# Performance work log

Measured on AMD Instinct MI355X. Metric: run time of the kernel, lower is better.

The kernel has to match this reference:

```python
import jax, jax.numpy as jnp
import numpy as np

BIG = 10000000.0

def heaviside(x):
    return (jnp.tanh(BIG * x) + 1.0) * 0.5

def interception(Prec, PET, INSC):
    INSC = jnp.clip(INSC * 5.0, 0.5, 5.0)
    IMAX = jnp.maximum(jnp.minimum(INSC, PET), 0.0)
    INT = jnp.maximum(jnp.minimum(IMAX, Prec), 0.0)
    INR = jnp.maximum(Prec - INT, 0.0)
    return INT, INR

def soil_moisture_store(SMS1, SMSC):
    SMSC = jnp.clip(SMSC * 500.0, 50.0, 500.0)
    return jnp.maximum(jnp.minimum(SMS1, SMSC), 0.0)

def soil_fluxes(PET, INT, INR, COEFF, SQ, SMSC, SUB, CRAK, SMS1):
    COEFF = jnp.clip(COEFF * 400.0, 50.0, 400.0)
    SQ = jnp.clip(SQ * 6.0, 0.0, 6.0)
    SMSC = jnp.clip(SMSC * 500.0, 50.0, 500.0)
    SUB = jnp.clip(SUB, 0.0, 1.0)
    CRAK = jnp.clip(CRAK, 0.0, 1.0)
    cap = COEFF * jnp.exp(-SQ * SMS1 / SMSC)
    RMO = jnp.maximum(heaviside(cap - INR) * INR + heaviside(INR - cap) * cap, 0.0)
    IRUN = jnp.maximum(INR - RMO, 0.0)
    SRUN = jnp.maximum(SUB * (SMS1 / SMSC) * RMO, 0.0)
    REC = jnp.maximum(CRAK * (SMS1 / SMSC) * (RMO - SRUN), 0.0)
    SMF = jnp.maximum(RMO - SRUN - REC, 0.0)
    POT = jnp.maximum(PET - INT, 0.0)
    r = 10.0 * SMS1 / SMSC
    ETS = jnp.maximum(heaviside(r - POT) * POT + heaviside(POT - r) * r, 0.0)
    return RMO, IRUN, SRUN, REC, SMF, ETS

def recharge_calculation(SMS1, SMSC, REC, SMF, ETS):
    SMSC = jnp.clip(SMSC * 500.0, 50.0, 500.0)
    s = SMS1 + SMF - ETS
    RECnew = heaviside(s - SMSC) * (REC + s - SMSC) + heaviside(SMSC - s) * REC
    return jnp.maximum(RECnew, 0.0)

def groundwaterstore(GW1, RecK):
    RecK = jnp.clip(RecK * 0.3, 0.003, 0.3)
    return jnp.maximum(heaviside(GW1) * (RecK * GW1), 0.0)

def _forward(inputs, INSC, COEFF, SQ, SMSC, SUB, CRAK, RecK):
    B, T, _ = inputs.shape
    xs = jnp.transpose(inputs, (1, 0, 2))  # (T, B, 2)

    def step(carry, x):
        SMS1, GW1 = carry  # each (B, 1)
        Prec, PET = x[:, 0:1], x[:, 1:2]
        INT, INR = interception(Prec, PET, INSC)
        SMS1c = soil_moisture_store(SMS1, SMSC)
        RMO, IRUN, SRUN, REC, SMF, ETS = soil_fluxes(PET, INT, INR, COEFF, SQ, SMSC, SUB, CRAK, SMS1c)
        next_SMS = SMS1c + jnp.clip(SMF - ETS, -100000.0, 100000.0)
        RECnew = recharge_calculation(SMS1c, SMSC, REC, SMF, ETS)
        BAS = groundwaterstore(GW1, RecK)
        next_GW = GW1 + jnp.clip(RECnew - BAS, -100000.0, 100000.0)
        return (next_SMS, next_GW), jnp.concatenate([next_SMS, next_GW], axis=1)

    init = (jnp.zeros((B, 1), inputs.dtype), jnp.zeros((B, 1), inputs.dtype))
    _, outs = jax.lax.scan(step, init, xs)  # (T, B, 2)
    outs = jnp.transpose(outs, (1, 0, 2))   # (B, T, 2)
    outs = jnp.roll(outs, shift=1, axis=1)  # state at step t-1 (wrap like tf.roll)
    SMS1 = outs[:, :, 0:1]
    GW1 = outs[:, :, 1:2]
    Prec = inputs[:, :, 0:1]
    PET = inputs[:, :, 1:2]
    INT, INR = interception(Prec, PET, INSC)
    SMS1 = soil_moisture_store(SMS1, SMSC)
    RMO, IRUN, SRUN, REC, SMF, ETS = soil_fluxes(PET, INT, INR, COEFF, SQ, SMSC, SUB, CRAK, SMS1)
    RECnew = recharge_calculation(SMS1, SMSC, REC, SMF, ETS)
    BAS = groundwaterstore(GW1, RecK)
    DR = jnp.maximum(SRUN + IRUN, 0.0)
    GD = jnp.maximum(BAS, 0.0)
    Q = jnp.maximum(DR + GD, 0.0)
    return Q  # (B, T, 1)


def setup_inputs() -> dict:
    key = jax.random.key(0)
    k1, = jax.random.split(key, 1)
    B, T = 4096, 1024
    # Prec in [0, 20) mm/day, PET in [0, 8) mm/day
    u = jax.random.uniform(k1, (B, T, 2), dtype=jnp.float32)
    scale = jnp.array([20.0, 8.0], dtype=jnp.float32)
    inputs = u * scale
    p = lambda v: jnp.full((1,), v, dtype=jnp.float32)
    return {
        "inputs": inputs,
        "INSC": p(0.5), "COEFF": p(0.5), "SQ": p(0.5), "SMSC": p(0.5),
        "SUB": p(0.5), "CRAK": p(0.5), "RecK": p(0.5),
    }


def reference(inputs, INSC, COEFF, SQ, SMSC, SUB, CRAK, RecK):
    return _forward(inputs, INSC, COEFF, SQ, SMSC, SUB, CRAK, RecK)
```

## Files before the change

kernel.cpp:

```cpp
#include <hip/hip_runtime.h>
#include <hip/hip_bf16.h>
#include <math.h>


struct P {
    float INSC, SMSC, RecK, g1, lc, k1, k2, k3, c2;
};

__device__ __forceinline__ P make_params(const float* pINSC, const float* pCOEFF,
                                         const float* pSQ,   const float* pSMSC,
                                         const float* pSUB,  const float* pCRAK,
                                         const float* pRecK) {
    P p;
    p.INSC      = fminf(fmaxf(pINSC[0]  * 5.0f,   0.5f),   5.0f);
    float COEFF = fminf(fmaxf(pCOEFF[0] * 400.0f, 50.0f),  400.0f);
    float SQ    = fminf(fmaxf(pSQ[0]    * 6.0f,   0.0f),   6.0f);
    p.SMSC      = fminf(fmaxf(pSMSC[0]  * 500.0f, 50.0f),  500.0f);
    float SUB   = fminf(fmaxf(pSUB[0],  0.0f), 1.0f);
    float CRAK  = fminf(fmaxf(pCRAK[0], 0.0f), 1.0f);
    p.RecK      = fminf(fmaxf(pRecK[0]  * 0.3f,   0.003f), 0.3f);
    p.g1 = 1.0f - p.RecK;
    p.lc = log2f(COEFF);
    float inv = 1.0f / p.SMSC;
    p.k1 = SUB * inv;
    p.k2 = CRAK * inv;
    p.k3 = 10.0f * inv;
    p.c2 = (-SQ * inv) * 1.44269504088896340736f;
    return p;
}

__device__ __forceinline__ float step(float Prec, float PET, float& sms, float& gw, const P& p) {
    float INT  = fminf(fminf(p.INSC, PET), Prec);
    float INR  = Prec - INT;
    float POT  = PET - INT;
    float S    = fminf(sms, p.SMSC);
    float u    = fmaf(-p.k1, S, 1.0f);
    float v    = fmaf(-p.k2, S, 1.0f);
    float ETS  = fminf(POT, p.k3 * S);
    float SmE  = S - ETS;
    float e    = exp2f(fmaf(p.c2, S, p.lc));
    float RMO  = fminf(INR, e);
    float w    = u * RMO;
    float s2   = fmaf(v, w, SmE);
    float SMF  = v * w;
    float REC  = w - SMF;
    float RECnew = REC + fmaxf(s2 - p.SMSC, 0.0f);
    float BAS  = p.RecK * gw;
    float Q    = (INR - w) + BAS;
    gw  = fmaf(p.g1, gw, RECnew);
    sms = s2;
    return Q;
}

__device__ __forceinline__ void stepw(float Prec, float PET, float& sms, float& gw, const P& p) {
    float INT  = fminf(fminf(p.INSC, PET), Prec);
    float INR  = Prec - INT;
    float POT  = PET - INT;
    float S    = fminf(sms, p.SMSC);
    float u    = fmaf(-p.k1, S, 1.0f);
    float v    = fmaf(-p.k2, S, 1.0f);
    float ETS  = fminf(POT, p.k3 * S);
    float SmE  = S - ETS;
    float e    = exp2f(fmaf(p.c2, S, p.lc));
    float RMO  = fminf(INR, e);
    float w    = u * RMO;
    float s2   = fmaf(v, w, SmE);
    float SMF  = v * w;
    float REC  = w - SMF;
    float RECnew = REC + fmaxf(s2 - p.SMSC, 0.0f);
    gw  = fmaf(p.g1, gw, RECnew);
    sms = s2;
}

__device__ __forceinline__ void dstep(float Prec, float PET,
                                      float& slo, float& shi, float& gw, const P& p) {
    float INT = fminf(fminf(p.INSC, PET), Prec);
    float INR = Prec - INT;
    float POT = PET - INT;
    {
        float S    = fminf(shi, p.SMSC);
        float u    = fmaf(-p.k1, S, 1.0f);
        float v    = fmaf(-p.k2, S, 1.0f);
        float ETS  = fminf(POT, p.k3 * S);
        float SmE  = S - ETS;
        float e    = exp2f(fmaf(p.c2, S, p.lc));
        float RMO  = fminf(INR, e);
        float w    = u * RMO;
        float s2   = fmaf(v, w, SmE);
        float SMF  = v * w;
        float REC  = w - SMF;
        float RECnew = REC + fmaxf(s2 - p.SMSC, 0.0f);
        gw  = fmaf(p.g1, gw, RECnew);
        shi = s2;
    }
    {
        float S    = fminf(slo, p.SMSC);
        float u    = fmaf(-p.k1, S, 1.0f);
        float v    = fmaf(-p.k2, S, 1.0f);
        float ETS  = fminf(POT, p.k3 * S);
        float SmE  = S - ETS;
        float e    = exp2f(fmaf(p.c2, S, p.lc));
        float RMO  = fminf(INR, e);
        float w    = u * RMO;
        slo = fmaf(v, w, SmE);
    }
}

#define MERGE_TOL 0.75f

template<int T, int NC, int W>
__global__ __launch_bounds__(64, 1)
void hir_pass1(const float* __restrict__ inputs,
               const float* __restrict__ pINSC,  const float* __restrict__ pCOEFF,
               const float* __restrict__ pSQ,    const float* __restrict__ pSMSC,
               const float* __restrict__ pSUB,   const float* __restrict__ pCRAK,
               const float* __restrict__ pRecK,
               float* __restrict__ out, float4* __restrict__ st, int B)
{
    int gid = blockIdx.x * blockDim.x + threadIdx.x;
    int b = gid % B;
    int c = gid / B;
    if (c >= NC) return;

    P p = make_params(pINSC, pCOEFF, pSQ, pSMSC, pSUB, pCRAK, pRecK);

    const float4* __restrict__ rp = (const float4*)(inputs + (size_t)b * (2 * T));
    float* __restrict__ orow = out + (size_t)b * T;

    constexpr int CH = T / NC;
    const int i1 = (c * CH) >> 1;
    int i0 = i1 - (W >> 1);
    const bool exact = (i0 <= 0);
    if (i0 < 0) i0 = 0;

    float slo = 0.0f, shi = exact ? 0.0f : p.SMSC, gw = 0.0f;

    const int nwb = (i1 - i0) >> 2;
    if (nwb > 0) {
        float4 A[4], Bq[4], C[4];
        #pragma unroll
        for (int j = 0; j < 4; ++j) A[j] = rp[i0 + j];
        {
            int k1b = (1 < nwb) ? 1 : 0;
            #pragma unroll
            for (int j = 0; j < 4; ++j) Bq[j] = rp[i0 + 4 * k1b + j];
        }
        if (exact) {
            for (int k = 0; k < nwb; ++k) {
                int kn = (k + 2 < nwb) ? (k + 2) : (nwb - 1);
                #pragma unroll
                for (int j = 0; j < 4; ++j) C[j] = rp[i0 + 4 * kn + j];
                #pragma unroll
                for (int j = 0; j < 4; ++j) {
                    stepw(A[j].x, A[j].y, shi, gw, p);
                    stepw(A[j].z, A[j].w, shi, gw, p);
                }
                #pragma unroll
                for (int j = 0; j < 4; ++j) { A[j] = Bq[j]; Bq[j] = C[j]; }
            }
            slo = shi;
        } else {
            for (int k = 0; k < nwb; ++k) {
                int kn = (k + 2 < nwb) ? (k + 2) : (nwb - 1);
                #pragma unroll
                for (int j = 0; j < 4; ++j) C[j] = rp[i0 + 4 * kn + j];
                #pragma unroll
                for (int j = 0; j < 4; ++j) {
                    dstep(A[j].x, A[j].y, slo, shi, gw, p);
                    dstep(A[j].z, A[j].w, slo, shi, gw, p);
                }
                #pragma unroll
                for (int j = 0; j < 4; ++j) { A[j] = Bq[j]; Bq[j] = C[j]; }
            }
        }
    }
    const bool merged = exact || ((shi - slo) <= MERGE_TOL);
    float sms = exact ? shi : (0.5f * (slo + shi));

    {
        constexpr int nmb = (CH / 2) / 4;
        float4 A[4], Bq[4], C[4];
        #pragma unroll
        for (int j = 0; j < 4; ++j) A[j] = rp[i1 + j];
        #pragma unroll
        for (int j = 0; j < 4; ++j) Bq[j] = rp[i1 + 4 + j];
        for (int k = 0; k < nmb; ++k) {
            int kn = (k + 2 < nmb) ? (k + 2) : (nmb - 1);
            #pragma unroll
            for (int j = 0; j < 4; ++j) C[j] = rp[i1 + 4 * kn + j];
            int ibase = i1 + 4 * k;
            #pragma unroll
            for (int j = 0; j < 4; ++j) {
                float qa = step(A[j].x, A[j].y, sms, gw, p);
                float qb = step(A[j].z, A[j].w, sms, gw, p);
                if (c == 0 && k == 0 && j == 0) {
                    orow[1] = qb;
                } else {
                    ((float2*)orow)[ibase + j] = make_float2(qa, qb);
                }
            }
            #pragma unroll
            for (int j = 0; j < 4; ++j) { A[j] = Bq[j]; Bq[j] = C[j]; }
        }
    }

    st[(size_t)c * B + b] = make_float4(sms, gw, merged ? 1.0f : 0.0f, 0.0f);

    if (c == NC - 1) {
        float4 f0 = rp[0];
        float ss = sms, gg = gw;
        orow[0] = step(f0.x, f0.y, ss, gg, p);
    }
}

template<int T, int NC>
__global__ __launch_bounds__(64, 1)
void hir_pass2(const float* __restrict__ inputs,
               const float* __restrict__ pINSC,  const float* __restrict__ pCOEFF,
               const float* __restrict__ pSQ,    const float* __restrict__ pSMSC,
               const float* __restrict__ pSUB,   const float* __restrict__ pCRAK,
               const float* __restrict__ pRecK,
               float* __restrict__ out, const float4* __restrict__ st, int B)
{
    int gid = blockIdx.x * blockDim.x + threadIdx.x;
    int b = gid % B;
    int c = gid / B;
    if (c >= NC) return;

    float4 sc = st[(size_t)c * B + b];
    if (sc.z != 0.0f) return;

    P p = make_params(pINSC, pCOEFF, pSQ, pSMSC, pSUB, pCRAK, pRecK);
    constexpr int CH = T / NC;

    const float4* __restrict__ rp = (const float4*)(inputs + (size_t)b * (2 * T));
    float* __restrict__ orow = out + (size_t)b * T;

    int m = c - 1;
    float4 sm = st[(size_t)m * B + b];
    while (sm.z == 0.0f) { --m; sm = st[(size_t)m * B + b]; }
    float sms = sm.x, gw = sm.y;

    {
        const int ia = ((m + 1) * CH) >> 1;
        const int ib = (c * CH) >> 1;
        if (ia < ib) {
            float4 cur = rp[ia];
            for (int i = ia; i < ib; ++i) {
                int ni = (i + 1 < ib) ? (i + 1) : i;
                float4 nxt = rp[ni];
                stepw(cur.x, cur.y, sms, gw, p);
                stepw(cur.z, cur.w, sms, gw, p);
                cur = nxt;
            }
        }
    }

    {
        const int i1 = (c * CH) >> 1;
        const int i2 = ((c + 1) * CH) >> 1;
        float4 cur = rp[i1];
        for (int i = i1; i < i2; ++i) {
            int ni = (i + 1 < i2) ? (i + 1) : i;
            float4 nxt = rp[ni];
            float qa = step(cur.x, cur.y, sms, gw, p);
            float qb = step(cur.z, cur.w, sms, gw, p);
            ((float2*)orow)[i] = make_float2(qa, qb);
            cur = nxt;
        }
    }

    if (c == NC - 1) {
        float4 f0 = rp[0];
        float ss = sms, gg = gw;
        orow[0] = step(f0.x, f0.y, ss, gg, p);
    }
}

template<int T>
__global__ __launch_bounds__(64, 1)
void hir_scan_kernel(const float* __restrict__ inputs,
                     const float* __restrict__ pINSC,  const float* __restrict__ pCOEFF,
                     const float* __restrict__ pSQ,    const float* __restrict__ pSMSC,
                     const float* __restrict__ pSUB,   const float* __restrict__ pCRAK,
                     const float* __restrict__ pRecK,
                     float* __restrict__ out, int B)
{
    int b = blockIdx.x * blockDim.x + threadIdx.x;
    if (b >= B) return;
    P p = make_params(pINSC, pCOEFF, pSQ, pSMSC, pSUB, pCRAK, pRecK);
    const float4* __restrict__ rp = (const float4*)(inputs + (size_t)b * (2 * T));
    float* __restrict__ orow = out + (size_t)b * T;
    float sms = 0.0f, gw = 0.0f;
    float4 cur = rp[0];
    const float P0 = cur.x, E0 = cur.y;
    constexpr int NI = T / 2;
    for (int i = 0; i < NI; ++i) {
        int ni = (i + 1 < NI) ? (i + 1) : i;
        float4 nxt = rp[ni];
        float qa = step(cur.x, cur.y, sms, gw, p);
        float qb = step(cur.z, cur.w, sms, gw, p);
        if (i == 0) { orow[1] = qb; }
        else        { ((float2*)orow)[i] = make_float2(qa, qb); }
        cur = nxt;
    }
    float ss = sms, gg = gw;
    orow[0] = step(P0, E0, ss, gg, p);
}

extern "C" void kernel_launch(void* const* d_in, const int* in_sizes, int n_in,
                              void* d_out, int out_size, void* d_ws, size_t ws_size,
                              hipStream_t stream) {
    (void)n_in; (void)out_size;
    constexpr int T  = 1024;
    constexpr int NC = 16;
    constexpr int W  = 320;
    const float* inputs = (const float*)d_in[0];
    const float* INSC   = (const float*)d_in[1];
    const float* COEFF  = (const float*)d_in[2];
    const float* SQ     = (const float*)d_in[3];
    const float* SMSC   = (const float*)d_in[4];
    const float* SUB    = (const float*)d_in[5];
    const float* CRAK   = (const float*)d_in[6];
    const float* RecK   = (const float*)d_in[7];
    float* out = (float*)d_out;

    int B = in_sizes[0] / (2 * T);
    size_t need = (size_t)B * NC * sizeof(float4);

    if (ws_size < need || (B % 64) != 0) {
        int blocks = (B + 63) / 64;
        hir_scan_kernel<T><<<dim3(blocks), dim3(64), 0, stream>>>(
            inputs, INSC, COEFF, SQ, SMSC, SUB, CRAK, RecK, out, B);
        return;
    }

    float4* st = (float4*)d_ws;
    long total = (long)B * NC;
    int blocks1 = (int)((total + 63) / 64);
    hir_pass1<T, NC, W><<<dim3(blocks1), dim3(64), 0, stream>>>(
        inputs, INSC, COEFF, SQ, SMSC, SUB, CRAK, RecK, out, st, B);
    int blocks2 = (int)((total + 63) / 64);
    hir_pass2<T, NC><<<dim3(blocks2), dim3(64), 0, stream>>>(
        inputs, INSC, COEFF, SQ, SMSC, SUB, CRAK, RecK, out, st, B);
}
```

Before: 120.8 us.

## Split dual-bound warmup across thread pairs and compact fixup work via atomic queue

The low/high bound warmup scans that one thread used to run together are now split across two lanes, which exchange results with a shuffle. This halves the per-thread serial latency of the warmup phase but doubles the thread count, and the main phase is computed redundantly on both lanes. Non-merged chunks are pushed onto a compacted work list with an atomicAdd, so the fixup kernel touches only those items instead of launching one thread per chunk. The change adds a memset and an atomic counter, and the second lane's main-phase work is wasted.

New measurement: 214.7 us. +77.7%, slower.

```diff
diff --git a/kernel.cpp b/kernel.cpp
--- a/kernel.cpp
+++ b/kernel.cpp
@@ -72,40 +72,6 @@
     sms = s2;
 }
 
-__device__ __forceinline__ void dstep(float Prec, float PET,
-                                      float& slo, float& shi, float& gw, const P& p) {
-    float INT = fminf(fminf(p.INSC, PET), Prec);
-    float INR = Prec - INT;
-    float POT = PET - INT;
-    {
-        float S    = fminf(shi, p.SMSC);
-        float u    = fmaf(-p.k1, S, 1.0f);
-        float v    = fmaf(-p.k2, S, 1.0f);
-        float ETS  = fminf(POT, p.k3 * S);
-        float SmE  = S - ETS;
-        float e    = exp2f(fmaf(p.c2, S, p.lc));
-        float RMO  = fminf(INR, e);
-        float w    = u * RMO;
-        float s2   = fmaf(v, w, SmE);
-        float SMF  = v * w;
-        float REC  = w - SMF;
-        float RECnew = REC + fmaxf(s2 - p.SMSC, 0.0f);
-        gw  = fmaf(p.g1, gw, RECnew);
-        shi = s2;
-    }
-    {
-        float S    = fminf(slo, p.SMSC);
-        float u    = fmaf(-p.k1, S, 1.0f);
-        float v    = fmaf(-p.k2, S, 1.0f);
-        float ETS  = fminf(POT, p.k3 * S);
-        float SmE  = S - ETS;
-        float e    = exp2f(fmaf(p.c2, S, p.lc));
-        float RMO  = fminf(INR, e);
-        float w    = u * RMO;
-        slo = fmaf(v, w, SmE);
-    }
-}
-
 #define MERGE_TOL 0.75f
 
 template<int T, int NC, int W>
@@ -115,11 +81,15 @@
                const float* __restrict__ pSQ,    const float* __restrict__ pSMSC,
                const float* __restrict__ pSUB,   const float* __restrict__ pCRAK,
                const float* __restrict__ pRecK,
-               float* __restrict__ out, float4* __restrict__ st, int B)
+               float* __restrict__ out, float4* __restrict__ st,
+               unsigned int* __restrict__ qcount, unsigned int* __restrict__ qitems,
+               int B)
 {
     int gid = blockIdx.x * blockDim.x + threadIdx.x;
-    int b = gid % B;
-    int c = gid / B;
+    int h  = gid & 1;
+    int pb = gid >> 1;
+    int b = pb % B;
+    int c = pb / B;
     if (c >= NC) return;
 
     P p = make_params(pINSC, pCOEFF, pSQ, pSMSC, pSUB, pCRAK, pRecK);
@@ -133,7 +103,8 @@
     const bool exact = (i0 <= 0);
     if (i0 < 0) i0 = 0;
 
-    float slo = 0.0f, shi = exact ? 0.0f : p.SMSC, gw = 0.0f;
+    float s  = exact ? 0.0f : (h ? 0.0f : p.SMSC);
+    float gw = 0.0f;
 
     const int nwb = (i1 - i0) >> 2;
     if (nwb > 0) {
@@ -145,37 +116,27 @@
             #pragma unroll
             for (int j = 0; j < 4; ++j) Bq[j] = rp[i0 + 4 * k1b + j];
         }
-        if (exact) {
-            for (int k = 0; k < nwb; ++k) {
-                int kn = (k + 2 < nwb) ? (k + 2) : (nwb - 1);
-                #pragma unroll
-                for (int j = 0; j < 4; ++j) C[j] = rp[i0 + 4 * kn + j];
-                #pragma unroll
-                for (int j = 0; j < 4; ++j) {
-                    stepw(A[j].x, A[j].y, shi, gw, p);
-                    stepw(A[j].z, A[j].w, shi, gw, p);
-                }
-                #pragma unroll
-                for (int j = 0; j < 4; ++j) { A[j] = Bq[j]; Bq[j] = C[j]; }
+        for (int k = 0; k < nwb; ++k) {
+            int kn = (k + 2 < nwb) ? (k + 2) : (nwb - 1);
+            #pragma unroll
+            for (int j = 0; j < 4; ++j) C[j] = rp[i0 + 4 * kn + j];
+            #pragma unroll
+            for (int j = 0; j < 4; ++j) {
+                stepw(A[j].x, A[j].y, s, gw, p);
+                stepw(A[j].z, A[j].w, s, gw, p);
             }
-            slo = shi;
-        } else {
-            for (int k = 0; k < nwb; ++k) {
-                int kn = (k + 2 < nwb) ? (k + 2) : (nwb - 1);
-                #pragma unroll
-                for (int j = 0; j < 4; ++j) C[j] = rp[i0 + 4 * kn + j];
-                #pragma unroll
-                for (int j = 0; j < 4; ++j) {
-                    dstep(A[j].x, A[j].y, slo, shi, gw, p);
-                    dstep(A[j].z, A[j].w, slo, shi, gw, p);
-                }
-                #pragma unroll
-                for (int j = 0; j < 4; ++j) { A[j] = Bq[j]; Bq[j] = C[j]; }
-            }
-        }
-    }
+            #pragma unroll
+            for (int j = 0; j < 4; ++j) { A[j] = Bq[j]; Bq[j] = C[j]; }
+        }
+    }
+
+    float so = __shfl_xor(s, 1);
+    float go = __shfl_xor(gw, 1);
+    float shi = h ? so : s;
+    float slo = h ? s : so;
+    gw = h ? go : gw;
     const bool merged = exact || ((shi - slo) <= MERGE_TOL);
-    float sms = exact ? shi : (0.5f * (slo + shi));
+    float sms = 0.5f * (slo + shi);
 
     {
         constexpr int nmb = (CH / 2) / 4;
@@ -193,10 +154,12 @@
             for (int j = 0; j < 4; ++j) {
                 float qa = step(A[j].x, A[j].y, sms, gw, p);
                 float qb = step(A[j].z, A[j].w, sms, gw, p);
-                if (c == 0 && k == 0 && j == 0) {
-                    orow[1] = qb;
-                } else {
-                    ((float2*)orow)[ibase + j] = make_float2(qa, qb);
+                if (!h) {
+                    if (c == 0 && k == 0 && j == 0) {
+                        orow[1] = qb;
+                    } else {
+                        ((float2*)orow)[ibase + j] = make_float2(qa, qb);
+                    }
                 }
             }
             #pragma unroll
@@ -204,76 +167,86 @@
         }
     }
 
-    st[(size_t)c * B + b] = make_float4(sms, gw, merged ? 1.0f : 0.0f, 0.0f);
-
-    if (c == NC - 1) {
-        float4 f0 = rp[0];
-        float ss = sms, gg = gw;
-        orow[0] = step(f0.x, f0.y, ss, gg, p);
+    if (!h) {
+        st[(size_t)c * B + b] = make_float4(sms, gw, merged ? 1.0f : 0.0f, 0.0f);
+        if (!merged) {
+            unsigned int idx = atomicAdd(qcount, 1u);
+            qitems[idx] = ((unsigned int)c << 24) | (unsigned int)b;
+        }
+        if (c == NC - 1) {
+            float4 f0 = rp[0];
+            float ss = sms, gg = gw;
+            orow[0] = step(f0.x, f0.y, ss, gg, p);
+        }
     }
 }
 
 template<int T, int NC>
 __global__ __launch_bounds__(64, 1)
-void hir_pass2(const float* __restrict__ inputs,
+void hir_fixup(const float* __restrict__ inputs,
                const float* __restrict__ pINSC,  const float* __restrict__ pCOEFF,
                const float* __restrict__ pSQ,    const float* __restrict__ pSMSC,
                const float* __restrict__ pSUB,   const float* __restrict__ pCRAK,
                const float* __restrict__ pRecK,
-               float* __restrict__ out, const float4* __restrict__ st, int B)
+               float* __restrict__ out, const float4* __restrict__ st,
+               const unsigned int* __restrict__ qcount,
+               const unsigned int* __restrict__ qitems, int B)
 {
     int gid = blockIdx.x * blockDim.x + threadIdx.x;
-    int b = gid % B;
-    int c = gid / B;
-    if (c >= NC) return;
-
-    float4 sc = st[(size_t)c * B + b];
-    if (sc.z != 0.0f) return;
+    int stride = gridDim.x * blockDim.x;
+    int n = (int)*qcount;
+    if (gid >= n) return;
 
     P p = make_params(pINSC, pCOEFF, pSQ, pSMSC, pSUB, pCRAK, pRecK);
     constexpr int CH = T / NC;
 
-    const float4* __restrict__ rp = (const float4*)(inputs + (size_t)b * (2 * T));
-    float* __restrict__ orow = out + (size_t)b * T;
-
-    int m = c - 1;
-    float4 sm = st[(size_t)m * B + b];
-    while (sm.z == 0.0f) { --m; sm = st[(size_t)m * B + b]; }
-    float sms = sm.x, gw = sm.y;
-
-    {
-        const int ia = ((m + 1) * CH) >> 1;
-        const int ib = (c * CH) >> 1;
-        if (ia < ib) {
-            float4 cur = rp[ia];
-            for (int i = ia; i < ib; ++i) {
-                int ni = (i + 1 < ib) ? (i + 1) : i;
+    for (int it = gid; it < n; it += stride) {
+        unsigned int item = qitems[it];
+        int b = (int)(item & 0xFFFFFFu);
+        int c = (int)(item >> 24);
+
+        const float4* __restrict__ rp = (const float4*)(inputs + (size_t)b * (2 * T));
+        float* __restrict__ orow = out + (size_t)b * T;
+
+        int m = c - 1;
+        float4 sm = st[(size_t)m * B + b];
+        while (sm.z == 0.0f) { --m; sm = st[(size_t)m * B + b]; }
+        float sms = sm.x, gw = sm.y;
+
+        {
+            const int ia = ((m + 1) * CH) >> 1;
+            const int ib = (c * CH) >> 1;
+            if (ia < ib) {
+                float4 cur = rp[ia];
+                for (int i = ia; i < ib; ++i) {
+                    int ni = (i + 1 < ib) ? (i + 1) : i;
+                    float4 nxt = rp[ni];
+                    stepw(cur.x, cur.y, sms, gw, p);
+                    stepw(cur.z, cur.w, sms, gw, p);
+                    cur = nxt;
+                }
+            }
+        }
+
+        {
+            const int i1 = (c * CH) >> 1;
+            const int i2 = ((c + 1) * CH) >> 1;
+            float4 cur = rp[i1];
+            for (int i = i1; i < i2; ++i) {
+                int ni = (i + 1 < i2) ? (i + 1) : i;
                 float4 nxt = rp[ni];
-                stepw(cur.x, cur.y, sms, gw, p);
-                stepw(cur.z, cur.w, sms, gw, p);
+                float qa = step(cur.x, cur.y, sms, gw, p);
+                float qb = step(cur.z, cur.w, sms, gw, p);
+                ((float2*)orow)[i] = make_float2(qa, qb);
                 cur = nxt;
             }
         }
-    }
-
-    {
-        const int i1 = (c * CH) >> 1;
-        const int i2 = ((c + 1) * CH) >> 1;
-        float4 cur = rp[i1];
-        for (int i = i1; i < i2; ++i) {
-            int ni = (i + 1 < i2) ? (i + 1) : i;
-            float4 nxt = rp[ni];
-            float qa = step(cur.x, cur.y, sms, gw, p);
-            float qb = step(cur.z, cur.w, sms, gw, p);
-            ((float2*)orow)[i] = make_float2(qa, qb);
-            cur = nxt;
-        }
-    }
-
-    if (c == NC - 1) {
-        float4 f0 = rp[0];
-        float ss = sms, gg = gw;
-        orow[0] = step(f0.x, f0.y, ss, gg, p);
+
+        if (c == NC - 1) {
+            float4 f0 = rp[0];
+            float ss = sms, gg = gw;
+            orow[0] = step(f0.x, f0.y, ss, gg, p);
+        }
     }
 }
 
@@ -326,7 +299,8 @@
     float* out = (float*)d_out;
 
     int B = in_sizes[0] / (2 * T);
-    size_t need = (size_t)B * NC * sizeof(float4);
+    size_t stBytes = (size_t)B * NC * sizeof(float4);
+    size_t need = stBytes + 64 + (size_t)B * NC * sizeof(unsigned int);
 
     if (ws_size < need || (B % 64) != 0) {
         int blocks = (B + 63) / 64;
@@ -336,11 +310,17 @@
     }
 
     float4* st = (float4*)d_ws;
-    long total = (long)B * NC;
+    unsigned int* qcount = (unsigned int*)((char*)d_ws + stBytes);
+    unsigned int* qitems = (unsigned int*)((char*)d_ws + stBytes + 64);
+
+    hipMemsetAsync(qcount, 0, sizeof(unsigned int), stream);
+
+    long total = 2L * B * NC;
     int blocks1 = (int)((total + 63) / 64);
     hir_pass1<T, NC, W><<<dim3(blocks1), dim3(64), 0, stream>>>(
-        inputs, INSC, COEFF, SQ, SMSC, SUB, CRAK, RecK, out, st, B);
-    int blocks2 = (int)((total + 63) / 64);
-    hir_pass2<T, NC><<<dim3(blocks2), dim3(64), 0, stream>>>(
-        inputs, INSC, COEFF, SQ, SMSC, SUB, CRAK, RecK, out, st, B);
-}
+        inputs, INSC, COEFF, SQ, SMSC, SUB, CRAK, RecK, out, st, qcount, qitems, B);
+
+    int blocks2 = 1024;
+    hir_fixup<T, NC><<<dim3(blocks2), dim3(64), 0, stream>>>(
+        inputs, INSC, COEFF, SQ, SMSC, SUB, CRAK, RecK, out, st, qcount, qitems, B);
+}
```

## Transpose inputs to time-major layout and compact unmerged chunks into a fixup queue

Applied to the files above, without the earlier changes.

Adds tiled shared-memory transpose kernels so the chunked scan reads inputs and writes outputs time-major, which makes adjacent threads (batch lanes) touch adjacent addresses and coalesces their accesses. Unmerged chunks are compacted with a ballot/atomic queue and repaired by a grid-stride fixup kernel rather than by launching one thread per chunk. The cost is two extra full-tensor transposes through the workspace, more kernel launches plus a memset, and strided uncoalesced accesses in the fixup path. It also reworks the legacy pass2 fallback to loop over chunks per batch row.

Result: slower. 145.9 us (+20.8%).

```diff
diff --git a/kernel.cpp b/kernel.cpp
--- a/kernel.cpp
+++ b/kernel.cpp
@@ -108,9 +108,237 @@
 
 #define MERGE_TOL 0.75f
 
+
+__global__ __launch_bounds__(256)
+void transpose_in(const float2* __restrict__ in, float2* __restrict__ tp,
+                  int B, int Tdim)
+{
+    __shared__ float2 tile[64][65];
+    int t0 = blockIdx.x * 64, b0 = blockIdx.y * 64;
+    int l = threadIdx.x & 63, w = threadIdx.x >> 6;
+    #pragma unroll
+    for (int j = 0; j < 16; ++j) {
+        int bb = w * 16 + j;
+        tile[l][bb] = in[(long)(b0 + bb) * Tdim + t0 + l];
+    }
+    __syncthreads();
+    #pragma unroll
+    for (int j = 0; j < 16; ++j) {
+        int tt = w * 16 + j;
+        tp[(long)(t0 + tt) * B + b0 + l] = tile[tt][l];
+    }
+}
+
+__global__ __launch_bounds__(256)
+void transpose_out(const float* __restrict__ qtp, float* __restrict__ out,
+                   int B, int Tdim)
+{
+    __shared__ float tile[64][65];
+    int t0 = blockIdx.x * 64, b0 = blockIdx.y * 64;
+    int l = threadIdx.x & 63, w = threadIdx.x >> 6;
+    #pragma unroll
+    for (int j = 0; j < 16; ++j) {
+        int tt = w * 16 + j;
+        tile[tt][l] = qtp[(long)(t0 + tt) * B + b0 + l];
+    }
+    __syncthreads();
+    #pragma unroll
+    for (int j = 0; j < 16; ++j) {
+        int bb = w * 16 + j;
+        out[(long)(b0 + bb) * Tdim + t0 + l] = tile[l][bb];
+    }
+}
+
+
 template<int T, int NC, int W>
 __global__ __launch_bounds__(64, 1)
-void hir_pass1(const float* __restrict__ inputs,
+void hir_pass1t(const float2* __restrict__ tp,
+                const float* __restrict__ pINSC,  const float* __restrict__ pCOEFF,
+                const float* __restrict__ pSQ,    const float* __restrict__ pSMSC,
+                const float* __restrict__ pSUB,   const float* __restrict__ pCRAK,
+                const float* __restrict__ pRecK,
+                float* __restrict__ qtp, float4* __restrict__ st, int B)
+{
+    int gid = blockIdx.x * blockDim.x + threadIdx.x;
+    int b = gid % B;
+    int c = gid / B;
+    if (c >= NC) return;
+
+    P p = make_params(pINSC, pCOEFF, pSQ, pSMSC, pSUB, pCRAK, pRecK);
+
+    const float2* __restrict__ col = tp + b;
+
+    constexpr int CH = T / NC;
+    const int t1 = c * CH;
+    int t0 = t1 - W;
+    const bool exact = (t0 <= 0);
+    if (t0 < 0) t0 = 0;
+
+    float slo = 0.0f, shi = exact ? 0.0f : p.SMSC, gw = 0.0f;
+
+    const int nwb = (t1 - t0) >> 3;
+    if (nwb > 0) {
+        float2 A[8], Bq[8], C[8];
+        #pragma unroll
+        for (int j = 0; j < 8; ++j) A[j] = col[(long)(t0 + j) * B];
+        {
+            int tB = t0 + ((1 < nwb) ? 8 : 0);
+            #pragma unroll
+            for (int j = 0; j < 8; ++j) Bq[j] = col[(long)(tB + j) * B];
+        }
+        if (exact) {
+            for (int k = 0; k < nwb; ++k) {
+                int kn = (k + 2 < nwb) ? (k + 2) : (nwb - 1);
+                #pragma unroll
+                for (int j = 0; j < 8; ++j) C[j] = col[(long)(t0 + 8 * kn + j) * B];
+                #pragma unroll
+                for (int j = 0; j < 8; ++j) stepw(A[j].x, A[j].y, shi, gw, p);
+                #pragma unroll
+                for (int j = 0; j < 8; ++j) { A[j] = Bq[j]; Bq[j] = C[j]; }
+            }
+            slo = shi;
+        } else {
+            for (int k = 0; k < nwb; ++k) {
+                int kn = (k + 2 < nwb) ? (k + 2) : (nwb - 1);
+                #pragma unroll
+                for (int j = 0; j < 8; ++j) C[j] = col[(long)(t0 + 8 * kn + j) * B];
+                #pragma unroll
+                for (int j = 0; j < 8; ++j) dstep(A[j].x, A[j].y, slo, shi, gw, p);
+                #pragma unroll
+                for (int j = 0; j < 8; ++j) { A[j] = Bq[j]; Bq[j] = C[j]; }
+            }
+        }
+    }
+    const bool merged = exact || ((shi - slo) <= MERGE_TOL);
+    float sms = exact ? shi : (0.5f * (slo + shi));
+
+    {
+        constexpr int nmb = CH / 8;
+        float2 A[8], Bq[8], C[8];
+        #pragma unroll
+        for (int j = 0; j < 8; ++j) A[j] = col[(long)(t1 + j) * B];
+        #pragma unroll
+        for (int j = 0; j < 8; ++j) Bq[j] = col[(long)(t1 + 8 + j) * B];
+        for (int k = 0; k < nmb; ++k) {
+            int kn = (k + 2 < nmb) ? (k + 2) : (nmb - 1);
+            #pragma unroll
+            for (int j = 0; j < 8; ++j) C[j] = col[(long)(t1 + 8 * kn + j) * B];
+            int tb = t1 + 8 * k;
+            #pragma unroll
+            for (int j = 0; j < 8; ++j) {
+                float q = step(A[j].x, A[j].y, sms, gw, p);
+                int t = tb + j;
+                if (!(c == 0 && t == 0)) {
+                    qtp[(long)t * B + b] = q;
+                }
+            }
+            #pragma unroll
+            for (int j = 0; j < 8; ++j) { A[j] = Bq[j]; Bq[j] = C[j]; }
+        }
+    }
+
+    st[(size_t)c * B + b] = make_float4(sms, gw, merged ? 1.0f : 0.0f, 0.0f);
+
+    if (c == NC - 1) {
+        float2 f0 = col[0];
+        float ss = sms, gg = gw;
+        qtp[b] = step(f0.x, f0.y, ss, gg, p);
+    }
+}
+
+
+__global__ __launch_bounds__(64)
+void build_queue(const float4* __restrict__ st, unsigned int* __restrict__ qcount,
+                 unsigned int* __restrict__ qitems, int n)
+{
+    int gid = blockIdx.x * blockDim.x + threadIdx.x;
+    bool un = false;
+    if (gid < n) un = (st[gid].z == 0.0f);
+    unsigned long long mask = __ballot(un);
+    int lane = threadIdx.x;
+    int cnt = __popcll(mask);
+    unsigned int base = 0;
+    if (lane == 0 && cnt) base = atomicAdd(qcount, (unsigned int)cnt);
+    base = (unsigned int)__shfl((int)base, 0);
+    if (un) {
+        int pre = __popcll(mask & ((1ull << lane) - 1ull));
+        qitems[base + pre] = (unsigned int)gid;
+    }
+}
+
+
+template<int T, int NC>
+__global__ __launch_bounds__(64)
+void hir_fixup(const float* __restrict__ inputs,
+               const float* __restrict__ pINSC,  const float* __restrict__ pCOEFF,
+               const float* __restrict__ pSQ,    const float* __restrict__ pSMSC,
+               const float* __restrict__ pSUB,   const float* __restrict__ pCRAK,
+               const float* __restrict__ pRecK,
+               float* __restrict__ qtp, const float4* __restrict__ st,
+               const unsigned int* __restrict__ qcount,
+               const unsigned int* __restrict__ qitems, int B)
+{
+    int gid = blockIdx.x * blockDim.x + threadIdx.x;
+    int stride = gridDim.x * blockDim.x;
+    int n = (int)*qcount;
+
+    P p = make_params(pINSC, pCOEFF, pSQ, pSMSC, pSUB, pCRAK, pRecK);
+    constexpr int CH = T / NC;
+
+    for (int it = gid; it < n; it += stride) {
+        unsigned int item = qitems[it];
+        int b = (int)(item % (unsigned int)B);
+        int c = (int)(item / (unsigned int)B);
+
+        const float4* __restrict__ rp = (const float4*)(inputs + (size_t)b * (2 * T));
+
+        int m = c - 1;
+        float4 sm = st[(size_t)m * B + b];
+        while (sm.z == 0.0f) { --m; sm = st[(size_t)m * B + b]; }
+        float sms = sm.x, gw = sm.y;
+
+        {
+            const int ia = ((m + 1) * CH) >> 1;
+            const int ib = (c * CH) >> 1;
+            if (ia < ib) {
+                float4 cur = rp[ia];
+                for (int i = ia; i < ib; ++i) {
+                    int ni = (i + 1 < ib) ? (i + 1) : i;
+                    float4 nxt = rp[ni];
+                    stepw(cur.x, cur.y, sms, gw, p);
+                    stepw(cur.z, cur.w, sms, gw, p);
+                    cur = nxt;
+                }
+            }
+        }
+
+        {
+            const int i1 = (c * CH) >> 1;
+            const int i2 = ((c + 1) * CH) >> 1;
+            float4 cur = rp[i1];
+            for (int i = i1; i < i2; ++i) {
+                int ni = (i + 1 < i2) ? (i + 1) : i;
+                float4 nxt = rp[ni];
+                float qa = step(cur.x, cur.y, sms, gw, p);
+                float qb = step(cur.z, cur.w, sms, gw, p);
+                qtp[(long)(2 * i) * B + b]     = qa;
+                qtp[(long)(2 * i + 1) * B + b] = qb;
+                cur = nxt;
+            }
+        }
+
+        if (c == NC - 1) {
+            float4 f0 = rp[0];
+            float ss = sms, gg = gw;
+            qtp[b] = step(f0.x, f0.y, ss, gg, p);
+        }
+    }
+}
+
+
+template<int T, int NC, int W>
+__global__ __launch_bounds__(64, 1)
+void hir_pass1_legacy(const float* __restrict__ inputs,
                const float* __restrict__ pINSC,  const float* __restrict__ pCOEFF,
                const float* __restrict__ pSQ,    const float* __restrict__ pSMSC,
                const float* __restrict__ pSUB,   const float* __restrict__ pCRAK,
@@ -215,20 +443,15 @@
 
 template<int T, int NC>
 __global__ __launch_bounds__(64, 1)
-void hir_pass2(const float* __restrict__ inputs,
+void hir_pass2_legacy(const float* __restrict__ inputs,
                const float* __restrict__ pINSC,  const float* __restrict__ pCOEFF,
                const float* __restrict__ pSQ,    const float* __restrict__ pSMSC,
                const float* __restrict__ pSUB,   const float* __restrict__ pCRAK,
                const float* __restrict__ pRecK,
                float* __restrict__ out, const float4* __restrict__ st, int B)
 {
-    int gid = blockIdx.x * blockDim.x + threadIdx.x;
-    int b = gid % B;
-    int c = gid / B;
-    if (c >= NC) return;
-
-    float4 sc = st[(size_t)c * B + b];
-    if (sc.z != 0.0f) return;
+    int b = blockIdx.x * blockDim.x + threadIdx.x;
+    if (b >= B) return;
 
     P p = make_params(pINSC, pCOEFF, pSQ, pSMSC, pSUB, pCRAK, pRecK);
     constexpr int CH = T / NC;
@@ -236,27 +459,16 @@
     const float4* __restrict__ rp = (const float4*)(inputs + (size_t)b * (2 * T));
     float* __restrict__ orow = out + (size_t)b * T;
 
-    int m = c - 1;
-    float4 sm = st[(size_t)m * B + b];
-    while (sm.z == 0.0f) { --m; sm = st[(size_t)m * B + b]; }
-    float sms = sm.x, gw = sm.y;
-
-    {
-        const int ia = ((m + 1) * CH) >> 1;
-        const int ib = (c * CH) >> 1;
-        if (ia < ib) {
-            float4 cur = rp[ia];
-            for (int i = ia; i < ib; ++i) {
-                int ni = (i + 1 < ib) ? (i + 1) : i;
-                float4 nxt = rp[ni];
-                stepw(cur.x, cur.y, sms, gw, p);
-                stepw(cur.z, cur.w, sms, gw, p);
-                cur = nxt;
-            }
-        }
-    }
-
-    {
+    float4 s0 = st[b];
+    float ex_s = s0.x, ex_g = s0.y;
+
+    for (int c = 1; c < NC; ++c) {
+        float4 sc = st[(size_t)c * B + b];
+        if (sc.z != 0.0f) {
+            ex_s = sc.x; ex_g = sc.y;
+            continue;
+        }
+        float sms = ex_s, gw = ex_g;
         const int i1 = (c * CH) >> 1;
         const int i2 = ((c + 1) * CH) >> 1;
         float4 cur = rp[i1];
@@ -268,12 +480,12 @@
             ((float2*)orow)[i] = make_float2(qa, qb);
             cur = nxt;
         }
-    }
-
-    if (c == NC - 1) {
-        float4 f0 = rp[0];
-        float ss = sms, gg = gw;
-        orow[0] = step(f0.x, f0.y, ss, gg, p);
+        ex_s = sms; ex_g = gw;
+        if (c == NC - 1) {
+            float4 f0 = rp[0];
+            float ss = sms, gg = gw;
+            orow[0] = step(f0.x, f0.y, ss, gg, p);
+        }
     }
 }
 
@@ -326,21 +538,53 @@
     float* out = (float*)d_out;
 
     int B = in_sizes[0] / (2 * T);
-    size_t need = (size_t)B * NC * sizeof(float4);
-
-    if (ws_size < need || (B % 64) != 0) {
-        int blocks = (B + 63) / 64;
-        hir_scan_kernel<T><<<dim3(blocks), dim3(64), 0, stream>>>(
-            inputs, INSC, COEFF, SQ, SMSC, SUB, CRAK, RecK, out, B);
+    size_t tpBytes  = (size_t)B * T * sizeof(float2);
+    size_t qtpBytes = (size_t)B * T * sizeof(float);
+    size_t stBytes  = (size_t)B * NC * sizeof(float4);
+    size_t qBytes   = (size_t)B * NC * sizeof(unsigned int);
+    size_t bigNeed  = tpBytes + qtpBytes + stBytes + 64 + qBytes;
+
+    if ((B % 64) == 0 && ws_size >= bigNeed) {
+        float2* tp = (float2*)d_ws;
+        float*  qtp = (float*)((char*)d_ws + tpBytes);
+        float4* st  = (float4*)((char*)d_ws + tpBytes + qtpBytes);
+        unsigned int* qcount = (unsigned int*)((char*)d_ws + tpBytes + qtpBytes + stBytes);
+        unsigned int* qitems = (unsigned int*)((char*)d_ws + tpBytes + qtpBytes + stBytes + 64);
+
+        hipMemsetAsync(qcount, 0, sizeof(unsigned int), stream);
+
+        transpose_in<<<dim3(T / 64, B / 64), dim3(256), 0, stream>>>(
+            (const float2*)inputs, tp, B, T);
+
+        long total = (long)B * NC;
+        int blocks1 = (int)((total + 63) / 64);
+        hir_pass1t<T, NC, W><<<dim3(blocks1), dim3(64), 0, stream>>>(
+            tp, INSC, COEFF, SQ, SMSC, SUB, CRAK, RecK, qtp, st, B);
+
+        build_queue<<<dim3(blocks1), dim3(64), 0, stream>>>(
+            st, qcount, qitems, (int)total);
+
+        hir_fixup<T, NC><<<dim3(1024), dim3(64), 0, stream>>>(
+            inputs, INSC, COEFF, SQ, SMSC, SUB, CRAK, RecK, qtp, st, qcount, qitems, B);
+
+        transpose_out<<<dim3(T / 64, B / 64), dim3(256), 0, stream>>>(
+            qtp, out, B, T);
         return;
     }
 
-    float4* st = (float4*)d_ws;
-    long total = (long)B * NC;
-    int blocks1 = (int)((total + 63) / 64);
-    hir_pass1<T, NC, W><<<dim3(blocks1), dim3(64), 0, stream>>>(
-        inputs, INSC, COEFF, SQ, SMSC, SUB, CRAK, RecK, out, st, B);
-    int blocks2 = (int)((total + 63) / 64);
-    hir_pass2<T, NC><<<dim3(blocks2), dim3(64), 0, stream>>>(
-        inputs, INSC, COEFF, SQ, SMSC, SUB, CRAK, RecK, out, st, B);
-}
+    if ((B % 64) == 0 && ws_size >= stBytes) {
+        float4* st = (float4*)d_ws;
+        long total = (long)B * NC;
+        int blocks1 = (int)((total + 63) / 64);
+        hir_pass1_legacy<T, NC, W><<<dim3(blocks1), dim3(64), 0, stream>>>(
+            inputs, INSC, COEFF, SQ, SMSC, SUB, CRAK, RecK, out, st, B);
+        int blocks2 = (B + 63) / 64;
+        hir_pass2_legacy<T, NC><<<dim3(blocks2), dim3(64), 0, stream>>>(
+            inputs, INSC, COEFF, SQ, SMSC, SUB, CRAK, RecK, out, st, B);
+        return;
+    }
+
+    int blocks = (B + 63) / 64;
+    hir_scan_kernel<T><<<dim3(blocks), dim3(64), 0, stream>>>(
+        inputs, INSC, COEFF, SQ, SMSC, SUB, CRAK, RecK, out, B);
+}
```

## Stage pass-1 outputs in LDS and write coalesced time-major rows

Applied to the files above, without the earlier changes.

Pass 1 now stores each thread's chunk of Q values into a padded shared-memory tile and, after a barrier, writes them out so that adjacent lanes write adjacent time steps of one batch row. Before, each lane wrote float2 values strided by a full row, which gave uncoalesced stores. The warm-up window W grows from 320 to 384 so more chunks can merge, at the cost of extra serial warm-up work. The fixup kernel drops its manual prefetch and gets relaxed launch bounds.

Result: slower. 123.8 us (+2.5%).

```diff
diff --git a/kernel.cpp b/kernel.cpp
--- a/kernel.cpp
+++ b/kernel.cpp
@@ -108,6 +108,7 @@
 
 #define MERGE_TOL 0.75f
 
+
 template<int T, int NC, int W>
 __global__ __launch_bounds__(64, 1)
 void hir_pass1(const float* __restrict__ inputs,
@@ -117,9 +118,11 @@
                const float* __restrict__ pRecK,
                float* __restrict__ out, float4* __restrict__ st, int B)
 {
-    int gid = blockIdx.x * blockDim.x + threadIdx.x;
-    int b = gid % B;
-    int c = gid / B;
+    __shared__ float lds_q[64][65];
+    const int l   = threadIdx.x;
+    const int gid = blockIdx.x * 64 + l;
+    const int b = gid % B;
+    const int c = gid / B;
     if (c >= NC) return;
 
     P p = make_params(pINSC, pCOEFF, pSQ, pSMSC, pSUB, pCRAK, pRecK);
@@ -188,16 +191,13 @@
             int kn = (k + 2 < nmb) ? (k + 2) : (nmb - 1);
             #pragma unroll
             for (int j = 0; j < 4; ++j) C[j] = rp[i1 + 4 * kn + j];
-            int ibase = i1 + 4 * k;
+            int tb = 8 * k;
             #pragma unroll
             for (int j = 0; j < 4; ++j) {
                 float qa = step(A[j].x, A[j].y, sms, gw, p);
                 float qb = step(A[j].z, A[j].w, sms, gw, p);
-                if (c == 0 && k == 0 && j == 0) {
-                    orow[1] = qb;
-                } else {
-                    ((float2*)orow)[ibase + j] = make_float2(qa, qb);
-                }
+                lds_q[tb + 2 * j][l]     = qa;
+                lds_q[tb + 2 * j + 1][l] = qb;
             }
             #pragma unroll
             for (int j = 0; j < 4; ++j) { A[j] = Bq[j]; Bq[j] = C[j]; }
@@ -206,25 +206,41 @@
 
     st[(size_t)c * B + b] = make_float4(sms, gw, merged ? 1.0f : 0.0f, 0.0f);
 
-    if (c == NC - 1) {
+    float q0 = 0.0f;
+    const bool hasq0 = (c == NC - 1);
+    if (hasq0) {
         float4 f0 = rp[0];
         float ss = sms, gg = gw;
-        orow[0] = step(f0.x, f0.y, ss, gg, p);
-    }
-}
+        q0 = step(f0.x, f0.y, ss, gg, p);
+    }
+
+    __syncthreads();
+
+    const int b0 = b - l;
+    const int t1 = c * CH;
+    const bool skip0 = (c == 0);
+    for (int j = 0; j < 64; ++j) {
+        float v = lds_q[l][j];
+        if (!skip0 || l > 0) {
+            out[(size_t)(b0 + j) * T + t1 + l] = v;
+        }
+    }
+    if (hasq0) orow[0] = q0;
+}
+
 
 template<int T, int NC>
-__global__ __launch_bounds__(64, 1)
-void hir_pass2(const float* __restrict__ inputs,
+__global__ __launch_bounds__(64)
+void hir_fixup(const float* __restrict__ inputs,
                const float* __restrict__ pINSC,  const float* __restrict__ pCOEFF,
                const float* __restrict__ pSQ,    const float* __restrict__ pSMSC,
                const float* __restrict__ pSUB,   const float* __restrict__ pCRAK,
                const float* __restrict__ pRecK,
                float* __restrict__ out, const float4* __restrict__ st, int B)
 {
-    int gid = blockIdx.x * blockDim.x + threadIdx.x;
-    int b = gid % B;
-    int c = gid / B;
+    const int gid = blockIdx.x * 64 + threadIdx.x;
+    const int b = gid % B;
+    const int c = gid / B;
     if (c >= NC) return;
 
     float4 sc = st[(size_t)c * B + b];
@@ -244,29 +260,21 @@
     {
         const int ia = ((m + 1) * CH) >> 1;
         const int ib = (c * CH) >> 1;
-        if (ia < ib) {
-            float4 cur = rp[ia];
-            for (int i = ia; i < ib; ++i) {
-                int ni = (i + 1 < ib) ? (i + 1) : i;
-                float4 nxt = rp[ni];
-                stepw(cur.x, cur.y, sms, gw, p);
-                stepw(cur.z, cur.w, sms, gw, p);
-                cur = nxt;
-            }
+        for (int i = ia; i < ib; ++i) {
+            float4 cur = rp[i];
+            stepw(cur.x, cur.y, sms, gw, p);
+            stepw(cur.z, cur.w, sms, gw, p);
         }
     }
 
     {
         const int i1 = (c * CH) >> 1;
         const int i2 = ((c + 1) * CH) >> 1;
-        float4 cur = rp[i1];
         for (int i = i1; i < i2; ++i) {
-            int ni = (i + 1 < i2) ? (i + 1) : i;
-            float4 nxt = rp[ni];
+            float4 cur = rp[i];
             float qa = step(cur.x, cur.y, sms, gw, p);
             float qb = step(cur.z, cur.w, sms, gw, p);
             ((float2*)orow)[i] = make_float2(qa, qb);
-            cur = nxt;
         }
     }
 
@@ -314,7 +322,7 @@
     (void)n_in; (void)out_size;
     constexpr int T  = 1024;
     constexpr int NC = 16;
-    constexpr int W  = 320;
+    constexpr int W  = 384;
     const float* inputs = (const float*)d_in[0];
     const float* INSC   = (const float*)d_in[1];
     const float* COEFF  = (const float*)d_in[2];
@@ -326,21 +334,20 @@
     float* out = (float*)d_out;
 
     int B = in_sizes[0] / (2 * T);
-    size_t need = (size_t)B * NC * sizeof(float4);
-
-    if (ws_size < need || (B % 64) != 0) {
-        int blocks = (B + 63) / 64;
-        hir_scan_kernel<T><<<dim3(blocks), dim3(64), 0, stream>>>(
-            inputs, INSC, COEFF, SQ, SMSC, SUB, CRAK, RecK, out, B);
+    size_t stBytes = (size_t)B * NC * sizeof(float4);
+
+    if ((B % 64) == 0 && ws_size >= stBytes) {
+        float4* st = (float4*)d_ws;
+        long total = (long)B * NC;
+        int blocks = (int)((total + 63) / 64);
+        hir_pass1<T, NC, W><<<dim3(blocks), dim3(64), 0, stream>>>(
+            inputs, INSC, COEFF, SQ, SMSC, SUB, CRAK, RecK, out, st, B);
+        hir_fixup<T, NC><<<dim3(blocks), dim3(64), 0, stream>>>(
+            inputs, INSC, COEFF, SQ, SMSC, SUB, CRAK, RecK, out, st, B);
         return;
     }
 
-    float4* st = (float4*)d_ws;
-    long total = (long)B * NC;
-    int blocks1 = (int)((total + 63) / 64);
-    hir_pass1<T, NC, W><<<dim3(blocks1), dim3(64), 0, stream>>>(
-        inputs, INSC, COEFF, SQ, SMSC, SUB, CRAK, RecK, out, st, B);
-    int blocks2 = (int)((total + 63) / 64);
-    hir_pass2<T, NC><<<dim3(blocks2), dim3(64), 0, stream>>>(
-        inputs, INSC, COEFF, SQ, SMSC, SUB, CRAK, RecK, out, st, B);
-}
+    int blocks = (B + 63) / 64;
+    hir_scan_kernel<T><<<dim3(blocks), dim3(64), 0, stream>>>(
+        inputs, INSC, COEFF, SQ, SMSC, SUB, CRAK, RecK, out, B);
+}
```
